# Kernel optimization log

Hardware: AMD Instinct MI355X
Metric: run time of the kernel (lower is better)

Reference implementation:

```python
import jax, jax.numpy as jnp
import numpy as np

NEG_INF = -1e30  # stand-in for float('-inf') that stays nan-free under softmax


def setup_inputs() -> dict:
    key = jax.random.key(0)
    k0, k1, k2, k3 = jax.random.split(key, 4)
    B, T, E, H = 4, 2048, 1024, 64
    X = jax.random.normal(k0, (B, T, E), dtype=jnp.float32)
    Wq = jax.random.normal(k1, (E, H), dtype=jnp.float32) * (E ** -0.5)
    Wk = jax.random.normal(k2, (E, H), dtype=jnp.float32) * (E ** -0.5)
    Wv = jax.random.normal(k3, (E, H), dtype=jnp.float32) * (E ** -0.5)
    return {"X": X, "Wq": Wq, "Wk": Wk, "Wv": Wv}


def reference(X, Wq, Wk, Wv):
    # X: [B, T, E]; W*: [E, H]
    B, T, C = X.shape
    Q = jnp.einsum('bte,eh->bth', X, Wq)
    K = jnp.einsum('bte,eh->bth', X, Wk)
    V = jnp.einsum('bte,eh->bth', X, Wv)
    # NOTE: original scales by emb_size**-0.5 (C), not head_size**-0.5
    wei = jnp.einsum('bqh,bkh->bqk', Q, K) * (C ** -0.5)  # [B, T, T]
    causal = jnp.tril(jnp.ones((T, T), dtype=bool))
    wei = jnp.where(causal, wei, NEG_INF)
    wei = jax.nn.softmax(wei, axis=-1)
    # dropout rate = 0.0 (eval-mode equivalent) -> identity
    out = jnp.einsum('bqk,bkh->bqh', wei, V)  # [B, T, H]
    return out
```

## Files before the change

kernel.cpp:

```cpp
#include <hip/hip_runtime.h>
#include <hip/hip_bf16.h>

constexpr int Bc = 4;
constexpr int Tc = 2048;
constexpr int Ec = 1024;
constexpr int Hc = 64;
constexpr float SCALE = 0.03125f;

typedef short  short8  __attribute__((ext_vector_type(8)));
typedef float  floatx4 __attribute__((ext_vector_type(4)));

__device__ __forceinline__ unsigned short f2bf(float f) {
    union { float f; unsigned int i; } x;
    x.f = f;
    unsigned int r = x.i + 0x7fffu + ((x.i >> 16) & 1u);
    return (unsigned short)(r >> 16);
}

__global__ __launch_bounds__(256) void prep_w(
    const float* __restrict__ Wq, const float* __restrict__ Wk,
    const float* __restrict__ Wv, unsigned short* __restrict__ Wt)
{
    const float* W = blockIdx.y == 0 ? Wq : (blockIdx.y == 1 ? Wk : Wv);
    unsigned short* D = Wt + (size_t)blockIdx.y * (Ec * Hc);
    const int i0 = blockIdx.x * 1024 + threadIdx.x * 4;
    const float4 f = *(const float4*)(W + i0);
    const float v[4] = {f.x, f.y, f.z, f.w};
    #pragma unroll
    for (int j = 0; j < 4; ++j) {
        const int i = i0 + j;
        D[(i & 63) * Ec + (i >> 6)] = f2bf(v[j]);
    }
}

__global__ __launch_bounds__(512, 2) void qkv_mfma9(
    const float* __restrict__ X, const unsigned short* __restrict__ Wt,
    unsigned short* __restrict__ Q, unsigned short* __restrict__ K,
    unsigned short* __restrict__ Vt)
{
    __shared__ __align__(16) unsigned short Xs[32][136];
    __shared__ __align__(16) unsigned short Ws[3][64][136];

    const int tid  = threadIdx.x;
    const int wv   = tid >> 6;
    const int lane = tid & 63;
    const int quad = lane >> 4;
    const int l16  = lane & 15;
    const int rowh = wv >> 2;
    const int wq   = wv & 3;
    const size_t row0 = (size_t)blockIdx.x * 32;

    floatx4 acc[3];
    #pragma unroll
    for (int j = 0; j < 3; ++j)
        #pragma unroll
        for (int r = 0; r < 4; ++r) acc[j][r] = 0.f;

    const int xrow = tid >> 4;
    const int xc4  = (tid & 15) * 4;

    float4 xreg[2];
    uint4  wreg[6];
    #pragma unroll
    for (int h = 0; h < 2; ++h)
        xreg[h] = *(const float4*)(X + (row0 + xrow) * Ec + h * 64 + xc4);
    #pragma unroll
    for (int j = 0; j < 6; ++j) {
        const int flat = tid + 512 * j;
        wreg[j] = *(const uint4*)(Wt + (flat >> 10) * 65536 +
                                  ((flat >> 4) & 63) * 1024 + (flat & 15) * 8);
    }

    for (int k0 = 0; k0 < Ec; k0 += 128) {
        __syncthreads();
        #pragma unroll
        for (int h = 0; h < 2; ++h) {
            uint2 p;
            p.x = (unsigned int)f2bf(xreg[h].x) | ((unsigned int)f2bf(xreg[h].y) << 16);
            p.y = (unsigned int)f2bf(xreg[h].z) | ((unsigned int)f2bf(xreg[h].w) << 16);
            *(uint2*)&Xs[xrow][h * 64 + xc4] = p;
        }
        #pragma unroll
        for (int j = 0; j < 6; ++j) {
            const int flat = tid + 512 * j;
            *(uint4*)&Ws[flat >> 10][(flat >> 4) & 63][(flat & 15) * 8] = wreg[j];
        }
        if (k0 + 128 < Ec) {
            #pragma unroll
            for (int h = 0; h < 2; ++h)
                xreg[h] = *(const float4*)(X + (row0 + xrow) * Ec + (k0 + 128) + h * 64 + xc4);
            #pragma unroll
            for (int j = 0; j < 6; ++j) {
                const int flat = tid + 512 * j;
                wreg[j] = *(const uint4*)(Wt + (flat >> 10) * 65536 +
                                          ((flat >> 4) & 63) * 1024 + (k0 + 128) + (flat & 15) * 8);
            }
        }
        __syncthreads();
        #pragma unroll
        for (int ks = 0; ks < 4; ++ks) {
            const short8 a = *(const short8*)&Xs[rowh * 16 + l16][ks * 32 + quad * 8];
            short8 b[3];
            #pragma unroll
            for (int j = 0; j < 3; ++j) {
                const int f = 3 * wq + j;
                b[j] = *(const short8*)&Ws[f >> 2][16 * (f & 3) + l16][ks * 32 + quad * 8];
            }
            #pragma unroll
            for (int j = 0; j < 3; ++j)
                acc[j] = __builtin_amdgcn_mfma_f32_16x16x32_bf16(a, b[j], acc[j], 0, 0, 0);
        }
    }

    const size_t rbase = row0 + rowh * 16;
    #pragma unroll
    for (int j = 0; j < 3; ++j) {
        const int f  = 3 * wq + j;
        const int mf = f >> 2, nf = f & 3;
        if (mf < 2) {
            unsigned short* O = mf == 0 ? Q : K;
            #pragma unroll
            for (int r = 0; r < 4; ++r) {
                float x = acc[j][r];
                if (!(x > -1.0e4f && x < 1.0e4f)) x = 11111.0f;
                O[(rbase + quad * 4 + r) * Hc + 16 * nf + l16] = f2bf(x);
            }
        } else {
            const size_t b  = rbase >> 11;
            const int    t0 = (int)(rbase & 2047) + quad * 4;
            unsigned short* VtB = Vt + b * ((size_t)Hc * Tc);
            unsigned int pk[2];
            #pragma unroll
            for (int half = 0; half < 2; ++half) {
                float x0 = acc[j][half * 2 + 0], x1 = acc[j][half * 2 + 1];
                if (!(x0 > -1.0e4f && x0 < 1.0e4f)) x0 = 11111.0f;
                if (!(x1 > -1.0e4f && x1 < 1.0e4f)) x1 = 11111.0f;
                pk[half] = (unsigned int)f2bf(x0) | ((unsigned int)f2bf(x1) << 16);
            }
            uint2 st; st.x = pk[0]; st.y = pk[1];
            *(uint2*)(VtB + (size_t)(16 * nf + l16) * Tc + t0) = st;
        }
    }
}

__global__ __launch_bounds__(512, 4) void attn_mfma6(
    const unsigned short* __restrict__ Q, const unsigned short* __restrict__ K,
    const unsigned short* __restrict__ Vt, float* __restrict__ Out)
{
    __shared__ __align__(16) unsigned short Pb[8][16][72];
    __shared__ __align__(16) float accS[8][16][64];
    __shared__ __align__(16) float lSr[8][16];

    const int tid  = threadIdx.x;
    const int wv   = tid >> 6;
    const int lane = tid & 63;
    const int quad = lane >> 4;
    const int l16  = lane & 15;
    const int id   = blockIdx.x + 128 * blockIdx.y;
    const int jj   = id & 255;
    const int qt   = (id < 256) ? (127 - (jj >> 2)) : (jj >> 2);
    const int b    = jj & 3;
    const int qend = qt * 16 + 16;
    const size_t base = (size_t)b * Tc * Hc;
    const unsigned short* VtB = Vt + (size_t)b * Hc * Tc;

    short8 aQ[2];
    #pragma unroll
    for (int ks = 0; ks < 2; ++ks)
        aQ[ks] = *(const short8*)(Q + base +
            (size_t)(qt * 16 + l16) * Hc + ks * 32 + quad * 8);

    floatx4 acc[4];
    float l_st[4];
    #pragma unroll
    for (int nh = 0; nh < 4; ++nh)
        #pragma unroll
        for (int r = 0; r < 4; ++r) acc[nh][r] = 0.f;
    #pragma unroll
    for (int r = 0; r < 4; ++r) l_st[r] = 0.f;

    for (int kb = wv * 64; kb < qend; kb += 512) {
        floatx4 s[4];
        #pragma unroll
        for (int ni = 0; ni < 4; ++ni)
            #pragma unroll
            for (int r = 0; r < 4; ++r) s[ni][r] = 0.f;
        #pragma unroll
        for (int ks = 0; ks < 2; ++ks) {
            short8 bk[4];
            #pragma unroll
            for (int ni = 0; ni < 4; ++ni)
                bk[ni] = *(const short8*)(K + base +
                    (size_t)(kb + 16 * ni + l16) * Hc + ks * 32 + quad * 8);
            __builtin_amdgcn_s_setprio(1);
            #pragma unroll
            for (int ni = 0; ni < 4; ++ni)
                s[ni] = __builtin_amdgcn_mfma_f32_16x16x32_bf16(aQ[ks], bk[ni], s[ni], 0, 0, 0);
            __builtin_amdgcn_s_setprio(0);
        }

        #pragma unroll
        for (int r = 0; r < 4; ++r) {
            const int qrow = qt * 16 + quad * 4 + r;
            #pragma unroll
            for (int ni = 0; ni < 4; ++ni) {
                const int kcol = kb + 16 * ni + l16;
                const float p = (kcol > qrow) ? 0.f : __expf(s[ni][r] * SCALE);
                s[ni][r] = p;
                l_st[r] += p;
            }
        }
        #pragma unroll
        for (int ni = 0; ni < 4; ++ni)
            #pragma unroll
            for (int r = 0; r < 4; ++r)
                Pb[wv][quad * 4 + r][16 * ni + l16] = f2bf(s[ni][r]);

        #pragma unroll
        for (int ks = 0; ks < 2; ++ks) {
            const short8 aP = *(const short8*)&Pb[wv][l16][ks * 32 + quad * 8];
            short8 bv[4];
            #pragma unroll
            for (int nh = 0; nh < 4; ++nh)
                bv[nh] = *(const short8*)(VtB +
                    (size_t)(16 * nh + l16) * Tc + kb + ks * 32 + quad * 8);
            __builtin_amdgcn_s_setprio(1);
            #pragma unroll
            for (int nh = 0; nh < 4; ++nh)
                acc[nh] = __builtin_amdgcn_mfma_f32_16x16x32_bf16(aP, bv[nh], acc[nh], 0, 0, 0);
            __builtin_amdgcn_s_setprio(0);
        }
    }

    #pragma unroll
    for (int nh = 0; nh < 4; ++nh)
        #pragma unroll
        for (int r = 0; r < 4; ++r)
            accS[wv][quad * 4 + r][16 * nh + l16] = acc[nh][r];
    #pragma unroll
    for (int r = 0; r < 4; ++r) {
        float v = l_st[r];
        v += __shfl_xor(v, 1);
        v += __shfl_xor(v, 2);
        v += __shfl_xor(v, 4);
        v += __shfl_xor(v, 8);
        l_st[r] = v;
    }
    if (l16 == 0)
        #pragma unroll
        for (int r = 0; r < 4; ++r)
            lSr[wv][quad * 4 + r] = l_st[r];
    __syncthreads();

    {
        const int q  = tid >> 5;
        const int h0 = (tid & 31) * 2;
        float denom = 0.f;
        #pragma unroll
        for (int w = 0; w < 8; ++w)
            denom += lSr[w][q];
        const float inv = 1.f / denom;
        float o0 = 0.f, o1 = 0.f;
        #pragma unroll
        for (int w = 0; w < 8; ++w) {
            const float2 v = *(const float2*)&accS[w][q][h0];
            o0 += v.x; o1 += v.y;
        }
        o0 *= inv; o1 *= inv;
        if (!(o0 > -1.0e5f && o0 < 1.0e5f)) o0 = 555.0f;
        if (!(o1 > -1.0e5f && o1 < 1.0e5f)) o1 = 555.0f;
        float2 st; st.x = o0; st.y = o1;
        *(float2*)(Out + base + (size_t)(qt * 16 + q) * Hc + h0) = st;
    }
}

extern "C" void kernel_launch(void* const* d_in, const int* in_sizes, int n_in,
                              void* d_out, int out_size, void* d_ws, size_t ws_size,
                              hipStream_t stream)
{
    const float* X  = (const float*)d_in[0];
    const float* Wq = (const float*)d_in[1];
    const float* Wk = (const float*)d_in[2];
    const float* Wv = (const float*)d_in[3];

    const size_t N = (size_t)Bc * Tc * Hc;
    unsigned short* Wt  = (unsigned short*)d_ws;
    unsigned short* Qws = Wt + 3 * (size_t)Ec * Hc;
    unsigned short* Kws = Qws + N;
    unsigned short* Vtw = Kws + N;

    prep_w<<<dim3(64, 3), dim3(256), 0, stream>>>(Wq, Wk, Wv, Wt);
    qkv_mfma9<<<dim3(256), dim3(512), 0, stream>>>(X, Wt, Qws, Kws, Vtw);
    attn_mfma6<<<dim3(128, 4), dim3(512), 0, stream>>>(
        Qws, Kws, Vtw, (float*)d_out);
}
```

Baseline: 130.1 us.

## Double-buffer QKV projection tiles with direct global-to-LDS weight loads

```diff
diff --git a/kernel.cpp b/kernel.cpp
--- a/kernel.cpp
+++ b/kernel.cpp
@@ -33,13 +33,13 @@
     }
 }
 
-__global__ __launch_bounds__(512, 2) void qkv_mfma9(
+__global__ __launch_bounds__(512, 2) void qkv_mfma11(
     const float* __restrict__ X, const unsigned short* __restrict__ Wt,
     unsigned short* __restrict__ Q, unsigned short* __restrict__ K,
     unsigned short* __restrict__ Vt)
 {
-    __shared__ __align__(16) unsigned short Xs[32][136];
-    __shared__ __align__(16) unsigned short Ws[3][64][136];
+    __shared__ __align__(16) unsigned short Xs[2][32][136];
+    __shared__ __align__(16) unsigned short Ws[2][3][64][128];
 
     const int tid  = threadIdx.x;
     const int wv   = tid >> 6;
@@ -59,56 +59,84 @@
     const int xrow = tid >> 4;
     const int xc4  = (tid & 15) * 4;
 
-    float4 xreg[2];
-    uint4  wreg[6];
-    #pragma unroll
-    for (int h = 0; h < 2; ++h)
-        xreg[h] = *(const float4*)(X + (row0 + xrow) * Ec + h * 64 + xc4);
-    #pragma unroll
-    for (int j = 0; j < 6; ++j) {
-        const int flat = tid + 512 * j;
-        wreg[j] = *(const uint4*)(Wt + (flat >> 10) * 65536 +
-                                  ((flat >> 4) & 63) * 1024 + (flat & 15) * 8);
-    }
-
-    for (int k0 = 0; k0 < Ec; k0 += 128) {
-        __syncthreads();
+    {
+        float4 xr[2];
+        #pragma unroll
+        for (int h = 0; h < 2; ++h)
+            xr[h] = *(const float4*)(X + (row0 + xrow) * Ec + h * 64 + xc4);
+        #pragma unroll
+        for (int j = 0; j < 6; ++j) {
+            const int flat  = tid + 512 * j;
+            const int which = flat >> 10;
+            const int r     = (flat >> 4) & 63;
+            const int chunk = (flat & 15) ^ (r & 7);
+            const unsigned short* src = Wt + which * 65536 + r * 1024 + chunk * 8;
+            char* dst = (char*)&Ws[0][0][0][0] + (wv * 64 + 512 * j) * 16;
+            __builtin_amdgcn_global_load_lds(
+                (const __attribute__((address_space(1))) unsigned int*)src,
+                (__attribute__((address_space(3))) unsigned int*)dst,
+                16, 0, 0);
+        }
         #pragma unroll
         for (int h = 0; h < 2; ++h) {
             uint2 p;
-            p.x = (unsigned int)f2bf(xreg[h].x) | ((unsigned int)f2bf(xreg[h].y) << 16);
-            p.y = (unsigned int)f2bf(xreg[h].z) | ((unsigned int)f2bf(xreg[h].w) << 16);
-            *(uint2*)&Xs[xrow][h * 64 + xc4] = p;
-        }
-        #pragma unroll
-        for (int j = 0; j < 6; ++j) {
-            const int flat = tid + 512 * j;
-            *(uint4*)&Ws[flat >> 10][(flat >> 4) & 63][(flat & 15) * 8] = wreg[j];
-        }
-        if (k0 + 128 < Ec) {
+            p.x = (unsigned int)f2bf(xr[h].x) | ((unsigned int)f2bf(xr[h].y) << 16);
+            p.y = (unsigned int)f2bf(xr[h].z) | ((unsigned int)f2bf(xr[h].w) << 16);
+            *(uint2*)&Xs[0][xrow][h * 64 + xc4] = p;
+        }
+        asm volatile("s_waitcnt vmcnt(0) lgkmcnt(0)" ::: "memory");
+        __builtin_amdgcn_s_barrier();
+    }
+
+    for (int t = 0; t < 8; ++t) {
+        const int cur = t & 1;
+        float4 xr[2];
+        if (t < 7) {
+            const int k1 = (t + 1) * 128;
             #pragma unroll
             for (int h = 0; h < 2; ++h)
-                xreg[h] = *(const float4*)(X + (row0 + xrow) * Ec + (k0 + 128) + h * 64 + xc4);
+                xr[h] = *(const float4*)(X + (row0 + xrow) * Ec + k1 + h * 64 + xc4);
             #pragma unroll
             for (int j = 0; j < 6; ++j) {
-                const int flat = tid + 512 * j;
-                wreg[j] = *(const uint4*)(Wt + (flat >> 10) * 65536 +
-                                          ((flat >> 4) & 63) * 1024 + (k0 + 128) + (flat & 15) * 8);
-            }
-        }
-        __syncthreads();
+                const int flat  = tid + 512 * j;
+                const int which = flat >> 10;
+                const int r     = (flat >> 4) & 63;
+                const int chunk = (flat & 15) ^ (r & 7);
+                const unsigned short* src = Wt + which * 65536 + r * 1024 + k1 + chunk * 8;
+                char* dst = (char*)&Ws[cur ^ 1][0][0][0] + (wv * 64 + 512 * j) * 16;
+                __builtin_amdgcn_global_load_lds(
+                    (const __attribute__((address_space(1))) unsigned int*)src,
+                    (__attribute__((address_space(3))) unsigned int*)dst,
+                    16, 0, 0);
+            }
+        }
+        __builtin_amdgcn_sched_barrier(0);
         #pragma unroll
         for (int ks = 0; ks < 4; ++ks) {
-            const short8 a = *(const short8*)&Xs[rowh * 16 + l16][ks * 32 + quad * 8];
+            const short8 a = *(const short8*)&Xs[cur][rowh * 16 + l16][ks * 32 + quad * 8];
             short8 b[3];
             #pragma unroll
             for (int j = 0; j < 3; ++j) {
-                const int f = 3 * wq + j;
-                b[j] = *(const short8*)&Ws[f >> 2][16 * (f & 3) + l16][ks * 32 + quad * 8];
+                const int f    = 3 * wq + j;
+                const int row  = 16 * (f & 3) + l16;
+                const int colb = (ks * 64 + quad * 16) ^ ((l16 & 7) << 4);
+                b[j] = *(const short8*)((const char*)&Ws[cur][f >> 2][row][0] + colb);
             }
             #pragma unroll
             for (int j = 0; j < 3; ++j)
                 acc[j] = __builtin_amdgcn_mfma_f32_16x16x32_bf16(a, b[j], acc[j], 0, 0, 0);
+        }
+        if (t < 7) {
+            __builtin_amdgcn_sched_barrier(0);
+            #pragma unroll
+            for (int h = 0; h < 2; ++h) {
+                uint2 p;
+                p.x = (unsigned int)f2bf(xr[h].x) | ((unsigned int)f2bf(xr[h].y) << 16);
+                p.y = (unsigned int)f2bf(xr[h].z) | ((unsigned int)f2bf(xr[h].w) << 16);
+                *(uint2*)&Xs[cur ^ 1][xrow][h * 64 + xc4] = p;
+            }
+            asm volatile("s_waitcnt vmcnt(0) lgkmcnt(0)" ::: "memory");
+            __builtin_amdgcn_s_barrier();
         }
     }
 
@@ -290,7 +318,7 @@
     unsigned short* Vtw = Kws + N;
 
     prep_w<<<dim3(64, 3), dim3(256), 0, stream>>>(Wq, Wk, Wv, Wt);
-    qkv_mfma9<<<dim3(256), dim3(512), 0, stream>>>(X, Wt, Qws, Kws, Vtw);
+    qkv_mfma11<<<dim3(256), dim3(512), 0, stream>>>(X, Wt, Qws, Kws, Vtw);
     attn_mfma6<<<dim3(128, 4), dim3(512), 0, stream>>>(
         Qws, Kws, Vtw, (float*)d_out);
 }
```

Result: faster. 106.2 us (-18.4%).
